# Optimization experiments

Measured on AMD Instinct MI355X. Metric: run time of the kernel, lower is better.

Reference implementation:

```python
import jax, jax.numpy as jnp
import numpy as np

N0, N1, N2, N3 = 1_000_000, 200_000, 20_000, 2_048
E0, E1, E2 = 2_000_000, 200_000, 20_480
IN, HID, OUT = 128, 256, 47


def setup_inputs() -> dict:
    key = jax.random.key(0)
    ks = jax.random.split(key, 16)
    d = {}
    d["x"] = jax.random.normal(ks[0], (N0, IN), dtype=jnp.float32)
    # block edge lists (src index into layer-input nodes, dst into layer-output nodes)
    d["src0"] = jax.random.randint(ks[1], (E0,), 0, N0)
    d["dst0"] = jax.random.randint(ks[2], (E0,), 0, N1)
    d["src1"] = jax.random.randint(ks[3], (E1,), 0, N1)
    d["dst1"] = jax.random.randint(ks[4], (E1,), 0, N2)
    d["src2"] = jax.random.randint(ks[5], (E2,), 0, N2)
    d["dst2"] = jax.random.randint(ks[6], (E2,), 0, N3)
    # SAGEConv params: fc_self / fc_neigh (bias-free) + shared bias
    def lin(k, fi, fo):
        return jax.random.normal(k, (fi, fo), dtype=jnp.float32) / np.sqrt(fi).astype(np.float32)
    d["W_self0"], d["W_neigh0"], d["b0"] = lin(ks[7], IN, HID), lin(ks[8], IN, HID), jnp.zeros((HID,), jnp.float32)
    d["W_self1"], d["W_neigh1"], d["b1"] = lin(ks[9], HID, HID), lin(ks[10], HID, HID), jnp.zeros((HID,), jnp.float32)
    d["W_self2"], d["W_neigh2"], d["b2"] = lin(ks[11], HID, OUT), lin(ks[12], HID, OUT), jnp.zeros((OUT,), jnp.float32)
    return d


def _sage_layer(h, src, dst, n_dst, W_self, W_neigh, b):
    # gather messages from src nodes, mean-reduce onto dst nodes
    msg = h[src]                                   # [E, d_in]
    agg = jax.ops.segment_sum(msg, dst, num_segments=n_dst)
    deg = jax.ops.segment_sum(jnp.ones((src.shape[0],), h.dtype), dst, num_segments=n_dst)
    h_neigh = agg / jnp.maximum(deg, 1.0)[:, None]
    h_dst = h[:n_dst]                              # DGL block convention: dst = first n_dst src nodes
    return h_dst @ W_self + h_neigh @ W_neigh + b


def reference(x, src0, dst0, src1, dst1, src2, dst2,
              W_self0, W_neigh0, b0, W_self1, W_neigh1, b1, W_self2, W_neigh2, b2):
    h = _sage_layer(x, src0, dst0, N1, W_self0, W_neigh0, b0)
    h = jax.nn.relu(h)  # dropout is identity in eval mode
    h = _sage_layer(h, src1, dst1, N2, W_self1, W_neigh1, b1)
    h = jax.nn.relu(h)
    h = _sage_layer(h, src2, dst2, N3, W_self2, W_neigh2, b2)
    return h
```

## Files before the change

kernel.cpp:

```cpp
#include <hip/hip_runtime.h>

#define N0_ 1000000
#define N1_ 200000
#define N2_ 20000
#define N3_ 2048
#define E0_ 2000000
#define E1_ 200000
#define E2_ 20480
#define IN_ 128
#define HID_ 256
#define OUT_ 47

#define NTOT_ (N1_ + N2_ + N3_)
#define ETOT_ (E0_ + E1_ + E2_)

typedef unsigned short u16;
typedef unsigned int u32;
typedef __attribute__((ext_vector_type(8))) short b16x8;
typedef __attribute__((ext_vector_type(4))) float f32x4;
typedef __attribute__((ext_vector_type(4))) u16 u16x4;
typedef __attribute__((ext_vector_type(8))) u16 u16x8;

__device__ __forceinline__ u16 f2b(float f) {
  u32 u = __builtin_bit_cast(u32, f);
  return (u16)((u + 0x7FFFu + ((u >> 16) & 1u)) >> 16);
}
__device__ __forceinline__ float b2f(u16 b) {
  return __builtin_bit_cast(float, (u32)b << 16);
}

static constexpr size_t OFF_CNT  = 0;
static constexpr size_t OFF_CUR  = 222048;
static constexpr size_t OFF_RPTR = 444096;
static constexpr size_t OFF_BSUM = 666176;
static constexpr size_t OFF_EIDS = 666304;
static constexpr size_t OFF_BT0  = 2886784;
static constexpr size_t OFF_BT1  = 2919552;
static constexpr size_t OFF_H1   = 2985088;
static constexpr size_t OFF_HN1  = 28585088;
static constexpr size_t OFF_H2   = 31145088;

__global__ __launch_bounds__(256) void prep(
    const int* __restrict__ dst0, const int* __restrict__ dst1,
    const int* __restrict__ dst2,
    const float* __restrict__ Ws0, const float* __restrict__ Wn0,
    const float* __restrict__ Ws1, const float* __restrict__ Wn1,
    int* __restrict__ cnt, u16* __restrict__ Bt0, u16* __restrict__ Bt1) {
  int t = blockIdx.x * 256 + threadIdx.x;
  if (t < E0_) { atomicAdd(&cnt[dst0[t]], 1); return; }
  t -= E0_;
  if (t < E1_) { atomicAdd(&cnt[N1_ + dst1[t]], 1); return; }
  t -= E1_;
  if (t < E2_) { atomicAdd(&cnt[N1_ + N2_ + dst2[t]], 1); return; }
  t -= E2_;
  if (t < 256 * 256) {
    int n = t & 255, k = t >> 8;
    float v = (k < IN_) ? Ws0[(size_t)k * 256 + n] : Wn0[(size_t)(k - IN_) * 256 + n];
    Bt0[(size_t)n * 256 + k] = f2b(v);
    return;
  }
  t -= 256 * 256;
  if (t < 256 * 512) {
    int n = t & 255, k = t >> 8;
    float v = (k < HID_) ? Ws1[(size_t)k * 256 + n] : Wn1[(size_t)(k - HID_) * 256 + n];
    Bt1[(size_t)n * 512 + k] = f2b(v);
  }
}

__global__ __launch_bounds__(256) void scan_local(const int* __restrict__ in,
                                                  int* __restrict__ out,
                                                  int* __restrict__ bsum, int n) {
  __shared__ int s[256];
  const int b = blockIdx.x, t = threadIdx.x;
  const int base = b * 2048 + t * 8;
  int v[8];
  int sum = 0;
#pragma unroll
  for (int i = 0; i < 8; i++) {
    int idx = base + i;
    int x = (idx < n) ? in[idx] : 0;
    v[i] = sum;
    sum += x;
  }
  s[t] = sum;
  __syncthreads();
  for (int off = 1; off < 256; off <<= 1) {
    int x = 0;
    if (t >= off) x = s[t - off];
    __syncthreads();
    if (t >= off) s[t] += x;
    __syncthreads();
  }
  const int texcl = s[t] - sum;
#pragma unroll
  for (int i = 0; i < 8; i++) {
    int idx = base + i;
    if (idx < n) out[idx] = texcl + v[i];
  }
  if (t == 255) bsum[b] = s[255];
}

__global__ __launch_bounds__(256) void scan_add(int* __restrict__ rptr,
                                                const int* __restrict__ bsum,
                                                int n, int E) {
  const int b = blockIdx.x, t = threadIdx.x;
  int add = 0;
  for (int i = 0; i < b; i++) add += bsum[i];
  const int base = b * 2048 + t * 8;
#pragma unroll
  for (int i = 0; i < 8; i++) {
    int idx = base + i;
    if (idx < n) rptr[idx] += add;
  }
  if (b == 0 && t == 0) rptr[n] = E;
}

__global__ __launch_bounds__(256) void csr_fill_all(
    const int* __restrict__ src0, const int* __restrict__ dst0,
    const int* __restrict__ src1, const int* __restrict__ dst1,
    const int* __restrict__ src2, const int* __restrict__ dst2,
    const int* __restrict__ rptr, int* __restrict__ cursor,
    int* __restrict__ eids) {
  int e = blockIdx.x * 256 + threadIdx.x;
  int s, b;
  if (e < E0_) { s = src0[e]; b = dst0[e]; }
  else if (e < E0_ + E1_) { s = src1[e - E0_]; b = N1_ + dst1[e - E0_]; }
  else if (e < ETOT_) { s = src2[e - E0_ - E1_]; b = N1_ + N2_ + dst2[e - E0_ - E1_]; }
  else return;
  int pos = rptr[b] + atomicAdd(&cursor[b], 1);
  eids[pos] = s;
}

__global__ __launch_bounds__(512, 4) void fused_sage0(
    const float* __restrict__ x, const int* __restrict__ eids,
    const int* __restrict__ rptr, const u16* __restrict__ Bt,
    const float* __restrict__ bias, u16* __restrict__ outp, int M) {
  __shared__ u16 Bs[256 * 64];
  __shared__ u16 As[128 * 64];
  __shared__ u16 HN[128 * 128];
  const int tid = threadIdx.x;
  const int lane = tid & 63;
  const int wv = tid >> 6;
  const int m0 = blockIdx.x * 128;

  {
    const int half = lane >> 5;
    const int colf = (lane & 31) * 4;
    for (int r = 0; r < 16; r++) {
      const int rl = wv * 16 + r;
      int rowg = m0 + rl; if (rowg >= M) rowg = M - 1;
      const int beg = rptr[rowg], end = rptr[rowg + 1];
      float a0 = 0.f, a1 = 0.f, a2 = 0.f, a3 = 0.f;
      for (int i = beg; i < end; i += 16) {
        int ids[8];
#pragma unroll
        for (int j = 0; j < 8; j++) {
          int idx = i + 2 * j + half;
          idx = idx < end ? idx : end - 1;
          ids[j] = eids[idx];
        }
        float4 v[8];
#pragma unroll
        for (int j = 0; j < 8; j++)
          v[j] = *reinterpret_cast<const float4*>(&x[(size_t)ids[j] * IN_ + colf]);
#pragma unroll
        for (int j = 0; j < 8; j++) {
          if (i + 2 * j + half < end) {
            a0 += v[j].x; a1 += v[j].y; a2 += v[j].z; a3 += v[j].w;
          }
        }
      }
      a0 += __shfl_xor(a0, 32, 64);
      a1 += __shfl_xor(a1, 32, 64);
      a2 += __shfl_xor(a2, 32, 64);
      a3 += __shfl_xor(a3, 32, 64);
      if (half == 0) {
        float inv = 1.0f / fmaxf((float)(end - beg), 1.0f);
        u32 p0 = (u32)f2b(a0 * inv) | ((u32)f2b(a1 * inv) << 16);
        u32 p1 = (u32)f2b(a2 * inv) | ((u32)f2b(a3 * inv) << 16);
        int byt = (rl * 256 + colf * 2) ^ ((rl & 7) << 4);
        u32* dp = reinterpret_cast<u32*>(reinterpret_cast<char*>(HN) + byt);
        dp[0] = p0; dp[1] = p1;
      }
    }
  }
  __syncthreads();

  const int wm = wv >> 2;
  const int wn = wv & 3;
  f32x4 acc[4][4];
#pragma unroll
  for (int m = 0; m < 4; m++)
#pragma unroll
    for (int n = 0; n < 4; n++) acc[m][n] = f32x4{0.f, 0.f, 0.f, 0.f};

#pragma unroll
  for (int kt = 0; kt < 256; kt += 64) {
    if (kt < 128) {
#pragma unroll
      for (int i = 0; i < 4; i++) {
        int e = tid + i * 512;
        int row = e >> 4;
        int c = (e & 15) * 4;
        int rowg = m0 + row; if (rowg >= M) rowg = M - 1;
        float4 v = *reinterpret_cast<const float4*>(&x[(size_t)rowg * IN_ + kt + c]);
        u32 p0 = (u32)f2b(v.x) | ((u32)f2b(v.y) << 16);
        u32 p1 = (u32)f2b(v.z) | ((u32)f2b(v.w) << 16);
        int byt = ((row * 64 + c) * 2) ^ ((row & 7) << 4);
        u32* dp = reinterpret_cast<u32*>(reinterpret_cast<char*>(As) + byt);
        dp[0] = p0; dp[1] = p1;
      }
    }
#pragma unroll
    for (int i = 0; i < 4; i++) {
      int e = tid + i * 512;
      int n = e >> 3;
      int ch = e & 7;
      u16x8 v = *reinterpret_cast<const u16x8*>(&Bt[(size_t)n * 256 + kt + ch * 8]);
      int byt = ((n * 64 + ch * 8) * 2) ^ ((n & 7) << 4);
      *reinterpret_cast<u16x8*>(reinterpret_cast<char*>(Bs) + byt) = v;
    }
    __syncthreads();
#pragma unroll
    for (int kk = 0; kk < 64; kk += 32) {
      const int ksl = kk + (lane >> 4) * 8;
      b16x8 a[4], b[4];
#pragma unroll
      for (int m = 0; m < 4; m++) {
        int row = wm * 64 + m * 16 + (lane & 15);
        if (kt < 128) {
          int byt = (row * 128 + ksl * 2) ^ ((row & 7) << 4);
          a[m] = *reinterpret_cast<const b16x8*>(reinterpret_cast<const char*>(As) + byt);
        } else {
          int byt = (row * 256 + (kt - 128 + ksl) * 2) ^ ((row & 7) << 4);
          a[m] = *reinterpret_cast<const b16x8*>(reinterpret_cast<const char*>(HN) + byt);
        }
      }
#pragma unroll
      for (int n = 0; n < 4; n++) {
        int row = wn * 64 + n * 16 + (lane & 15);
        int byt = (row * 128 + ksl * 2) ^ ((row & 7) << 4);
        b[n] = *reinterpret_cast<const b16x8*>(reinterpret_cast<const char*>(Bs) + byt);
      }
#pragma unroll
      for (int m = 0; m < 4; m++)
#pragma unroll
        for (int n = 0; n < 4; n++)
          acc[m][n] = __builtin_amdgcn_mfma_f32_16x16x32_bf16(a[m], b[n], acc[m][n], 0, 0, 0);
    }
    __syncthreads();
  }
  float bv[4];
#pragma unroll
  for (int n = 0; n < 4; n++) bv[n] = bias[wn * 64 + n * 16 + (lane & 15)];
#pragma unroll
  for (int m = 0; m < 4; m++) {
    int rowb = m0 + wm * 64 + m * 16 + ((lane >> 4) << 2);
#pragma unroll
    for (int r = 0; r < 4; r++) {
      int row = rowb + r;
      if (row < M) {
#pragma unroll
        for (int n = 0; n < 4; n++) {
          float v = acc[m][n][r] + bv[n];
          v = fmaxf(v, 0.0f);
          outp[(size_t)row * 256 + wn * 64 + n * 16 + (lane & 15)] = f2b(v);
        }
      }
    }
  }
}

__global__ __launch_bounds__(256) void agg1(const u16* __restrict__ h,
                                            const int* __restrict__ eids,
                                            const int* __restrict__ rptr,
                                            u16* __restrict__ out, int M) {
  int wid = (blockIdx.x * 256 + threadIdx.x) >> 6;
  int lane = threadIdx.x & 63;
  if (wid >= M) return;
  const int beg = rptr[wid], end = rptr[wid + 1];
  const int half = lane >> 5;
  const int col = (lane & 31) * 8;
  float a[8];
#pragma unroll
  for (int j = 0; j < 8; j++) a[j] = 0.f;
  for (int i = beg; i < end; i += 16) {
    int ids[8];
#pragma unroll
    for (int j = 0; j < 8; j++) {
      int idx = i + 2 * j + half;
      idx = idx < end ? idx : end - 1;
      ids[j] = eids[idx];
    }
    u16x8 v[8];
#pragma unroll
    for (int j = 0; j < 8; j++)
      v[j] = *reinterpret_cast<const u16x8*>(&h[(size_t)ids[j] * HID_ + col]);
#pragma unroll
    for (int j = 0; j < 8; j++) {
      if (i + 2 * j + half < end) {
#pragma unroll
        for (int c = 0; c < 8; c++) a[c] += b2f(v[j][c]);
      }
    }
  }
#pragma unroll
  for (int c = 0; c < 8; c++) a[c] += __shfl_xor(a[c], 32, 64);
  if (half == 0) {
    float inv = 1.0f / fmaxf((float)(end - beg), 1.0f);
    u16x8 o;
#pragma unroll
    for (int c = 0; c < 8; c++) o[c] = f2b(a[c] * inv);
    *reinterpret_cast<u16x8*>(&out[(size_t)wid * HID_ + col]) = o;
  }
}

template <int KSELF>
__global__ __launch_bounds__(512) void sage_gemm_mfma(
    const u16* __restrict__ A0, const u16* __restrict__ A1,
    const u16* __restrict__ Bt, const float* __restrict__ bias,
    u16* __restrict__ outp, int M) {
  constexpr int KTOT = 2 * KSELF;
  __shared__ u16 As[128 * 64];
  __shared__ u16 Bs[256 * 64];
  const int tid = threadIdx.x;
  const int lane = tid & 63;
  const int w = tid >> 6;
  const int wm = w >> 2;
  const int wn = w & 3;
  const int m0 = blockIdx.x * 128;

  f32x4 acc[4][4];
#pragma unroll
  for (int m = 0; m < 4; m++)
#pragma unroll
    for (int n = 0; n < 4; n++) acc[m][n] = f32x4{0.f, 0.f, 0.f, 0.f};

  for (int kt = 0; kt < KTOT; kt += 64) {
    const u16* src; int ksrc;
    if (kt < KSELF) { src = A0; ksrc = kt; }
    else            { src = A1; ksrc = kt - KSELF; }
#pragma unroll
    for (int i = 0; i < 2; i++) {
      int e = tid + i * 512;
      int row = e >> 3;
      int ch = e & 7;
      int rowg = m0 + row; if (rowg >= M) rowg = M - 1;
      u16x8 v = *reinterpret_cast<const u16x8*>(&src[(size_t)rowg * KSELF + ksrc + ch * 8]);
      int byt = ((row * 64 + ch * 8) * 2) ^ ((row & 7) << 4);
      *reinterpret_cast<u16x8*>(reinterpret_cast<char*>(As) + byt) = v;
    }
#pragma unroll
    for (int i = 0; i < 4; i++) {
      int e = tid + i * 512;
      int n = e >> 3;
      int ch = e & 7;
      u16x8 v = *reinterpret_cast<const u16x8*>(&Bt[(size_t)n * KTOT + kt + ch * 8]);
      int byt = ((n * 64 + ch * 8) * 2) ^ ((n & 7) << 4);
      *reinterpret_cast<u16x8*>(reinterpret_cast<char*>(Bs) + byt) = v;
    }
    __syncthreads();
#pragma unroll
    for (int kk = 0; kk < 64; kk += 32) {
      const int kb = (kk + (lane >> 4) * 8) * 2;
      b16x8 a[4], b[4];
#pragma unroll
      for (int m = 0; m < 4; m++) {
        int row = wm * 64 + m * 16 + (lane & 15);
        int byt = (row * 128 + kb) ^ ((row & 7) << 4);
        a[m] = *reinterpret_cast<const b16x8*>(reinterpret_cast<const char*>(As) + byt);
      }
#pragma unroll
      for (int n = 0; n < 4; n++) {
        int row = wn * 64 + n * 16 + (lane & 15);
        int byt = (row * 128 + kb) ^ ((row & 7) << 4);
        b[n] = *reinterpret_cast<const b16x8*>(reinterpret_cast<const char*>(Bs) + byt);
      }
#pragma unroll
      for (int m = 0; m < 4; m++)
#pragma unroll
        for (int n = 0; n < 4; n++)
          acc[m][n] = __builtin_amdgcn_mfma_f32_16x16x32_bf16(a[m], b[n], acc[m][n], 0, 0, 0);
    }
    __syncthreads();
  }
  float bv[4];
#pragma unroll
  for (int n = 0; n < 4; n++) bv[n] = bias[wn * 64 + n * 16 + (lane & 15)];
#pragma unroll
  for (int m = 0; m < 4; m++) {
    int rowb = m0 + wm * 64 + m * 16 + ((lane >> 4) << 2);
#pragma unroll
    for (int r = 0; r < 4; r++) {
      int row = rowb + r;
      if (row < M) {
#pragma unroll
        for (int n = 0; n < 4; n++) {
          float v = acc[m][n][r] + bv[n];
          v = fmaxf(v, 0.0f);
          outp[(size_t)row * 256 + wn * 64 + n * 16 + (lane & 15)] = f2b(v);
        }
      }
    }
  }
}

__global__ __launch_bounds__(64) void fused_out(
    const u16* __restrict__ h, const int* __restrict__ eids,
    const int* __restrict__ rptr, const float* __restrict__ Ws,
    const float* __restrict__ Wn, const float* __restrict__ bias,
    float* __restrict__ out) {
  __shared__ float As[512];
  const int row = blockIdx.x;
  const int t = threadIdx.x;
  u16x4 a = *reinterpret_cast<const u16x4*>(&h[(size_t)row * 256 + t * 4]);
#pragma unroll
  for (int j = 0; j < 4; j++) As[t * 4 + j] = b2f(a[j]);
  const int beg = rptr[row], end = rptr[row + 1];
  float s0 = 0.f, s1 = 0.f, s2 = 0.f, s3 = 0.f;
  for (int i = beg; i < end; i += 4) {
    int i1 = (i + 1 < end) ? i + 1 : i;
    int i2 = (i + 2 < end) ? i + 2 : i;
    int i3 = (i + 3 < end) ? i + 3 : i;
    int e0 = eids[i], e1 = eids[i1], e2 = eids[i2], e3 = eids[i3];
    u16x4 v0 = *reinterpret_cast<const u16x4*>(&h[(size_t)e0 * 256 + t * 4]);
    u16x4 v1 = *reinterpret_cast<const u16x4*>(&h[(size_t)e1 * 256 + t * 4]);
    u16x4 v2 = *reinterpret_cast<const u16x4*>(&h[(size_t)e2 * 256 + t * 4]);
    u16x4 v3 = *reinterpret_cast<const u16x4*>(&h[(size_t)e3 * 256 + t * 4]);
    s0 += b2f(v0[0]); s1 += b2f(v0[1]); s2 += b2f(v0[2]); s3 += b2f(v0[3]);
    if (i + 1 < end) { s0 += b2f(v1[0]); s1 += b2f(v1[1]); s2 += b2f(v1[2]); s3 += b2f(v1[3]); }
    if (i + 2 < end) { s0 += b2f(v2[0]); s1 += b2f(v2[1]); s2 += b2f(v2[2]); s3 += b2f(v2[3]); }
    if (i + 3 < end) { s0 += b2f(v3[0]); s1 += b2f(v3[1]); s2 += b2f(v3[2]); s3 += b2f(v3[3]); }
  }
  float inv = 1.0f / fmaxf((float)(end - beg), 1.0f);
  As[256 + t * 4 + 0] = s0 * inv;
  As[256 + t * 4 + 1] = s1 * inv;
  As[256 + t * 4 + 2] = s2 * inv;
  As[256 + t * 4 + 3] = s3 * inv;
  __syncthreads();
  if (t < OUT_) {
    float s = bias[t];
#pragma unroll 8
    for (int k = 0; k < 256; k++) s = fmaf(As[k], Ws[k * 47 + t], s);
#pragma unroll 8
    for (int k = 0; k < 256; k++) s = fmaf(As[256 + k], Wn[k * 47 + t], s);
    out[(size_t)row * 47 + t] = s;
  }
}

extern "C" void kernel_launch(void* const* d_in, const int* in_sizes, int n_in,
                              void* d_out, int out_size, void* d_ws, size_t ws_size,
                              hipStream_t stream) {
  const float* x      = (const float*)d_in[0];
  const int*   src0   = (const int*)d_in[1];
  const int*   dst0   = (const int*)d_in[2];
  const int*   src1   = (const int*)d_in[3];
  const int*   dst1   = (const int*)d_in[4];
  const int*   src2   = (const int*)d_in[5];
  const int*   dst2   = (const int*)d_in[6];
  const float* Wself0 = (const float*)d_in[7];
  const float* Wneigh0= (const float*)d_in[8];
  const float* b0     = (const float*)d_in[9];
  const float* Wself1 = (const float*)d_in[10];
  const float* Wneigh1= (const float*)d_in[11];
  const float* b1     = (const float*)d_in[12];
  const float* Wself2 = (const float*)d_in[13];
  const float* Wneigh2= (const float*)d_in[14];
  const float* b2     = (const float*)d_in[15];

  int* wsi   = (int*)d_ws;
  int* cnt   = wsi + OFF_CNT;
  int* cursor= wsi + OFF_CUR;
  int* rptr  = wsi + OFF_RPTR;
  int* bsum  = wsi + OFF_BSUM;
  int* eids  = wsi + OFF_EIDS;
  u16* Bt0   = (u16*)(wsi + OFF_BT0);
  u16* Bt1   = (u16*)(wsi + OFF_BT1);
  u16* H1    = (u16*)(wsi + OFF_H1);
  u16* HN1   = (u16*)(wsi + OFF_HN1);
  u16* H2    = (u16*)(wsi + OFF_H2);
  float* out = (float*)d_out;

  hipMemsetAsync(cnt, 0, (size_t)(2 * NTOT_) * 4, stream);

  {
    int total = ETOT_ + 256 * 256 + 256 * 512;
    prep<<<(total + 255) / 256, 256, 0, stream>>>(
        dst0, dst1, dst2, Wself0, Wneigh0, Wself1, Wneigh1, cnt, Bt0, Bt1);
  }
  {
    const int nb = (NTOT_ + 2047) / 2048;
    scan_local<<<nb, 256, 0, stream>>>(cnt, rptr, bsum, NTOT_);
    scan_add<<<nb, 256, 0, stream>>>(rptr, bsum, NTOT_, ETOT_);
    csr_fill_all<<<(ETOT_ + 255) / 256, 256, 0, stream>>>(
        src0, dst0, src1, dst1, src2, dst2, rptr, cursor, eids);
  }

  fused_sage0<<<(N1_ + 127) / 128, 512, 0, stream>>>(x, eids, rptr, Bt0, b0, H1, N1_);

  agg1<<<(N2_ + 3) / 4, 256, 0, stream>>>(H1, eids, rptr + N1_, HN1, N2_);
  sage_gemm_mfma<HID_><<<(N2_ + 127) / 128, 512, 0, stream>>>(H1, HN1, Bt1, b1, H2, N2_);

  fused_out<<<N3_, 64, 0, stream>>>(H2, eids, rptr + N1_ + N2_, Wself2, Wneigh2, b2, out);
}
```

Baseline: 580.4 us.

## Split layer-0 fused kernel into separate aggregation and GEMM kernels

The fused gather-plus-GEMM kernel for layer 0 is replaced by a standalone one-wave-per-row aggregation kernel that writes bf16 neighbour means to a new workspace buffer, followed by the generic MFMA GEMM, which gains a template path that converts fp32 self features on the fly. The GEMM also stops staging weights through shared memory and reads B fragments straight from global memory, cutting LDS use. This aims to raise occupancy and parallelism in the gather phase, which the 512-thread fused block serialized. The cost is an extra bf16 round trip of the 200k×128 aggregate through HBM and uncached, possibly less coalesced B loads.

```diff
diff --git a/kernel.cpp b/kernel.cpp
--- a/kernel.cpp
+++ b/kernel.cpp
@@ -36,9 +36,10 @@
 static constexpr size_t OFF_EIDS = 666304;
 static constexpr size_t OFF_BT0  = 2886784;
 static constexpr size_t OFF_BT1  = 2919552;
-static constexpr size_t OFF_H1   = 2985088;
-static constexpr size_t OFF_HN1  = 28585088;
-static constexpr size_t OFF_H2   = 31145088;
+static constexpr size_t OFF_HN0  = 2985088;
+static constexpr size_t OFF_H1   = 15785088;
+static constexpr size_t OFF_HN1  = 41385088;
+static constexpr size_t OFF_H2   = 43945088;
 
 __global__ __launch_bounds__(256) void prep(
     const int* __restrict__ dst0, const int* __restrict__ dst1,
@@ -131,143 +132,46 @@
   eids[pos] = s;
 }
 
-__global__ __launch_bounds__(512, 4) void fused_sage0(
-    const float* __restrict__ x, const int* __restrict__ eids,
-    const int* __restrict__ rptr, const u16* __restrict__ Bt,
-    const float* __restrict__ bias, u16* __restrict__ outp, int M) {
-  __shared__ u16 Bs[256 * 64];
-  __shared__ u16 As[128 * 64];
-  __shared__ u16 HN[128 * 128];
-  const int tid = threadIdx.x;
-  const int lane = tid & 63;
-  const int wv = tid >> 6;
-  const int m0 = blockIdx.x * 128;
-
-  {
-    const int half = lane >> 5;
-    const int colf = (lane & 31) * 4;
-    for (int r = 0; r < 16; r++) {
-      const int rl = wv * 16 + r;
-      int rowg = m0 + rl; if (rowg >= M) rowg = M - 1;
-      const int beg = rptr[rowg], end = rptr[rowg + 1];
-      float a0 = 0.f, a1 = 0.f, a2 = 0.f, a3 = 0.f;
-      for (int i = beg; i < end; i += 16) {
-        int ids[8];
-#pragma unroll
-        for (int j = 0; j < 8; j++) {
-          int idx = i + 2 * j + half;
-          idx = idx < end ? idx : end - 1;
-          ids[j] = eids[idx];
-        }
-        float4 v[8];
-#pragma unroll
-        for (int j = 0; j < 8; j++)
-          v[j] = *reinterpret_cast<const float4*>(&x[(size_t)ids[j] * IN_ + colf]);
-#pragma unroll
-        for (int j = 0; j < 8; j++) {
-          if (i + 2 * j + half < end) {
-            a0 += v[j].x; a1 += v[j].y; a2 += v[j].z; a3 += v[j].w;
-          }
-        }
-      }
-      a0 += __shfl_xor(a0, 32, 64);
-      a1 += __shfl_xor(a1, 32, 64);
-      a2 += __shfl_xor(a2, 32, 64);
-      a3 += __shfl_xor(a3, 32, 64);
-      if (half == 0) {
-        float inv = 1.0f / fmaxf((float)(end - beg), 1.0f);
-        u32 p0 = (u32)f2b(a0 * inv) | ((u32)f2b(a1 * inv) << 16);
-        u32 p1 = (u32)f2b(a2 * inv) | ((u32)f2b(a3 * inv) << 16);
-        int byt = (rl * 256 + colf * 2) ^ ((rl & 7) << 4);
-        u32* dp = reinterpret_cast<u32*>(reinterpret_cast<char*>(HN) + byt);
-        dp[0] = p0; dp[1] = p1;
-      }
-    }
-  }
-  __syncthreads();
-
-  const int wm = wv >> 2;
-  const int wn = wv & 3;
-  f32x4 acc[4][4];
-#pragma unroll
-  for (int m = 0; m < 4; m++)
-#pragma unroll
-    for (int n = 0; n < 4; n++) acc[m][n] = f32x4{0.f, 0.f, 0.f, 0.f};
-
-#pragma unroll
-  for (int kt = 0; kt < 256; kt += 64) {
-    if (kt < 128) {
-#pragma unroll
-      for (int i = 0; i < 4; i++) {
-        int e = tid + i * 512;
-        int row = e >> 4;
-        int c = (e & 15) * 4;
-        int rowg = m0 + row; if (rowg >= M) rowg = M - 1;
-        float4 v = *reinterpret_cast<const float4*>(&x[(size_t)rowg * IN_ + kt + c]);
-        u32 p0 = (u32)f2b(v.x) | ((u32)f2b(v.y) << 16);
-        u32 p1 = (u32)f2b(v.z) | ((u32)f2b(v.w) << 16);
-        int byt = ((row * 64 + c) * 2) ^ ((row & 7) << 4);
-        u32* dp = reinterpret_cast<u32*>(reinterpret_cast<char*>(As) + byt);
-        dp[0] = p0; dp[1] = p1;
-      }
-    }
-#pragma unroll
-    for (int i = 0; i < 4; i++) {
-      int e = tid + i * 512;
-      int n = e >> 3;
-      int ch = e & 7;
-      u16x8 v = *reinterpret_cast<const u16x8*>(&Bt[(size_t)n * 256 + kt + ch * 8]);
-      int byt = ((n * 64 + ch * 8) * 2) ^ ((n & 7) << 4);
-      *reinterpret_cast<u16x8*>(reinterpret_cast<char*>(Bs) + byt) = v;
-    }
-    __syncthreads();
-#pragma unroll
-    for (int kk = 0; kk < 64; kk += 32) {
-      const int ksl = kk + (lane >> 4) * 8;
-      b16x8 a[4], b[4];
-#pragma unroll
-      for (int m = 0; m < 4; m++) {
-        int row = wm * 64 + m * 16 + (lane & 15);
-        if (kt < 128) {
-          int byt = (row * 128 + ksl * 2) ^ ((row & 7) << 4);
-          a[m] = *reinterpret_cast<const b16x8*>(reinterpret_cast<const char*>(As) + byt);
-        } else {
-          int byt = (row * 256 + (kt - 128 + ksl) * 2) ^ ((row & 7) << 4);
-          a[m] = *reinterpret_cast<const b16x8*>(reinterpret_cast<const char*>(HN) + byt);
-        }
-      }
-#pragma unroll
-      for (int n = 0; n < 4; n++) {
-        int row = wn * 64 + n * 16 + (lane & 15);
-        int byt = (row * 128 + ksl * 2) ^ ((row & 7) << 4);
-        b[n] = *reinterpret_cast<const b16x8*>(reinterpret_cast<const char*>(Bs) + byt);
-      }
-#pragma unroll
-      for (int m = 0; m < 4; m++)
-#pragma unroll
-        for (int n = 0; n < 4; n++)
-          acc[m][n] = __builtin_amdgcn_mfma_f32_16x16x32_bf16(a[m], b[n], acc[m][n], 0, 0, 0);
-    }
-    __syncthreads();
-  }
-  float bv[4];
-#pragma unroll
-  for (int n = 0; n < 4; n++) bv[n] = bias[wn * 64 + n * 16 + (lane & 15)];
-#pragma unroll
-  for (int m = 0; m < 4; m++) {
-    int rowb = m0 + wm * 64 + m * 16 + ((lane >> 4) << 2);
-#pragma unroll
-    for (int r = 0; r < 4; r++) {
-      int row = rowb + r;
-      if (row < M) {
-#pragma unroll
-        for (int n = 0; n < 4; n++) {
-          float v = acc[m][n][r] + bv[n];
-          v = fmaxf(v, 0.0f);
-          outp[(size_t)row * 256 + wn * 64 + n * 16 + (lane & 15)] = f2b(v);
-        }
-      }
-    }
+__global__ __launch_bounds__(256) void agg0(const float* __restrict__ h,
+                                            const int* __restrict__ eids,
+                                            const int* __restrict__ rptr,
+                                            u16* __restrict__ out, int M) {
+  int wid = (blockIdx.x * 256 + threadIdx.x) >> 6;
+  int lane = threadIdx.x & 63;
+  if (wid >= M) return;
+  const int beg = rptr[wid], end = rptr[wid + 1];
+  const int half = lane >> 5;
+  const int col = (lane & 31) * 4;
+  float a0 = 0.f, a1 = 0.f, a2 = 0.f, a3 = 0.f;
+  for (int i = beg; i < end; i += 16) {
+    int ids[8];
+#pragma unroll
+    for (int j = 0; j < 8; j++) {
+      int idx = i + 2 * j + half;
+      idx = idx < end ? idx : end - 1;
+      ids[j] = eids[idx];
+    }
+    float4 v[8];
+#pragma unroll
+    for (int j = 0; j < 8; j++)
+      v[j] = *reinterpret_cast<const float4*>(&h[(size_t)ids[j] * IN_ + col]);
+#pragma unroll
+    for (int j = 0; j < 8; j++) {
+      if (i + 2 * j + half < end) {
+        a0 += v[j].x; a1 += v[j].y; a2 += v[j].z; a3 += v[j].w;
+      }
+    }
+  }
+  a0 += __shfl_xor(a0, 32, 64);
+  a1 += __shfl_xor(a1, 32, 64);
+  a2 += __shfl_xor(a2, 32, 64);
+  a3 += __shfl_xor(a3, 32, 64);
+  if (half == 0) {
+    float inv = 1.0f / fmaxf((float)(end - beg), 1.0f);
+    u16x4 o;
+    o[0] = f2b(a0 * inv); o[1] = f2b(a1 * inv);
+    o[2] = f2b(a2 * inv); o[3] = f2b(a3 * inv);
+    *reinterpret_cast<u16x4*>(&out[(size_t)wid * IN_ + col]) = o;
   }
 }
 
@@ -315,14 +219,13 @@
   }
 }
 
-template <int KSELF>
+template <int KSELF, bool A0F32>
 __global__ __launch_bounds__(512) void sage_gemm_mfma(
-    const u16* __restrict__ A0, const u16* __restrict__ A1,
+    const void* __restrict__ A0v, const u16* __restrict__ A1,
     const u16* __restrict__ Bt, const float* __restrict__ bias,
     u16* __restrict__ outp, int M) {
   constexpr int KTOT = 2 * KSELF;
   __shared__ u16 As[128 * 64];
-  __shared__ u16 Bs[256 * 64];
   const int tid = threadIdx.x;
   const int lane = tid & 63;
   const int w = tid >> 6;
@@ -337,44 +240,51 @@
     for (int n = 0; n < 4; n++) acc[m][n] = f32x4{0.f, 0.f, 0.f, 0.f};
 
   for (int kt = 0; kt < KTOT; kt += 64) {
-    const u16* src; int ksrc;
-    if (kt < KSELF) { src = A0; ksrc = kt; }
-    else            { src = A1; ksrc = kt - KSELF; }
-#pragma unroll
-    for (int i = 0; i < 2; i++) {
-      int e = tid + i * 512;
-      int row = e >> 3;
-      int ch = e & 7;
-      int rowg = m0 + row; if (rowg >= M) rowg = M - 1;
-      u16x8 v = *reinterpret_cast<const u16x8*>(&src[(size_t)rowg * KSELF + ksrc + ch * 8]);
-      int byt = ((row * 64 + ch * 8) * 2) ^ ((row & 7) << 4);
-      *reinterpret_cast<u16x8*>(reinterpret_cast<char*>(As) + byt) = v;
-    }
-#pragma unroll
-    for (int i = 0; i < 4; i++) {
-      int e = tid + i * 512;
-      int n = e >> 3;
-      int ch = e & 7;
-      u16x8 v = *reinterpret_cast<const u16x8*>(&Bt[(size_t)n * KTOT + kt + ch * 8]);
-      int byt = ((n * 64 + ch * 8) * 2) ^ ((n & 7) << 4);
-      *reinterpret_cast<u16x8*>(reinterpret_cast<char*>(Bs) + byt) = v;
+    if (A0F32 && kt < KSELF) {
+      const float* A0 = (const float*)A0v;
+#pragma unroll
+      for (int i = 0; i < 4; i++) {
+        int e = tid + i * 512;
+        int row = e >> 4;
+        int c = (e & 15) * 4;
+        int rowg = m0 + row; if (rowg >= M) rowg = M - 1;
+        float4 v = *reinterpret_cast<const float4*>(&A0[(size_t)rowg * KSELF + kt + c]);
+        u32 p0 = (u32)f2b(v.x) | ((u32)f2b(v.y) << 16);
+        u32 p1 = (u32)f2b(v.z) | ((u32)f2b(v.w) << 16);
+        int byt = ((row * 64 + c) * 2) ^ ((row & 7) << 4);
+        u32* dp = reinterpret_cast<u32*>(reinterpret_cast<char*>(As) + byt);
+        dp[0] = p0; dp[1] = p1;
+      }
+    } else {
+      const u16* src; int ksrc;
+      if (!A0F32 && kt < KSELF) { src = (const u16*)A0v; ksrc = kt; }
+      else                      { src = A1;              ksrc = kt - KSELF; }
+#pragma unroll
+      for (int i = 0; i < 2; i++) {
+        int e = tid + i * 512;
+        int row = e >> 3;
+        int ch = e & 7;
+        int rowg = m0 + row; if (rowg >= M) rowg = M - 1;
+        u16x8 v = *reinterpret_cast<const u16x8*>(&src[(size_t)rowg * KSELF + ksrc + ch * 8]);
+        int byt = ((row * 64 + ch * 8) * 2) ^ ((row & 7) << 4);
+        *reinterpret_cast<u16x8*>(reinterpret_cast<char*>(As) + byt) = v;
+      }
     }
     __syncthreads();
 #pragma unroll
     for (int kk = 0; kk < 64; kk += 32) {
-      const int kb = (kk + (lane >> 4) * 8) * 2;
+      const int ksl = kk + (lane >> 4) * 8;
       b16x8 a[4], b[4];
+#pragma unroll
+      for (int n = 0; n < 4; n++) {
+        int nrow = wn * 64 + n * 16 + (lane & 15);
+        b[n] = *reinterpret_cast<const b16x8*>(&Bt[(size_t)nrow * KTOT + kt + ksl]);
+      }
 #pragma unroll
       for (int m = 0; m < 4; m++) {
         int row = wm * 64 + m * 16 + (lane & 15);
-        int byt = (row * 128 + kb) ^ ((row & 7) << 4);
+        int byt = (row * 128 + ksl * 2) ^ ((row & 7) << 4);
         a[m] = *reinterpret_cast<const b16x8*>(reinterpret_cast<const char*>(As) + byt);
-      }
-#pragma unroll
-      for (int n = 0; n < 4; n++) {
-        int row = wn * 64 + n * 16 + (lane & 15);
-        int byt = (row * 128 + kb) ^ ((row & 7) << 4);
-        b[n] = *reinterpret_cast<const b16x8*>(reinterpret_cast<const char*>(Bs) + byt);
       }
 #pragma unroll
       for (int m = 0; m < 4; m++)
@@ -476,6 +386,7 @@
   int* eids  = wsi + OFF_EIDS;
   u16* Bt0   = (u16*)(wsi + OFF_BT0);
   u16* Bt1   = (u16*)(wsi + OFF_BT1);
+  u16* HN0   = (u16*)(wsi + OFF_HN0);
   u16* H1    = (u16*)(wsi + OFF_H1);
   u16* HN1   = (u16*)(wsi + OFF_HN1);
   u16* H2    = (u16*)(wsi + OFF_H2);
@@ -496,10 +407,13 @@
         src0, dst0, src1, dst1, src2, dst2, rptr, cursor, eids);
   }
 
-  fused_sage0<<<(N1_ + 127) / 128, 512, 0, stream>>>(x, eids, rptr, Bt0, b0, H1, N1_);
+  agg0<<<(N1_ + 3) / 4, 256, 0, stream>>>(x, eids, rptr, HN0, N1_);
+  sage_gemm_mfma<IN_, true><<<(N1_ + 127) / 128, 512, 0, stream>>>(
+      x, HN0, Bt0, b0, H1, N1_);
 
   agg1<<<(N2_ + 3) / 4, 256, 0, stream>>>(H1, eids, rptr + N1_, HN1, N2_);
-  sage_gemm_mfma<HID_><<<(N2_ + 127) / 128, 512, 0, stream>>>(H1, HN1, Bt1, b1, H2, N2_);
+  sage_gemm_mfma<HID_, false><<<(N2_ + 127) / 128, 512, 0, stream>>>(
+      H1, HN1, Bt1, b1, H2, N2_);
 
   fused_out<<<N3_, 64, 0, stream>>>(H2, eids, rptr + N1_ + N2_, Wself2, Wneigh2, b2, out);
 }
```

After: 550.4 us. 1.05x faster.
